# Kernel optimization log

Measured on AMD Instinct MI355X. Metric: run time of the kernel, lower is better.

The kernel has to match this reference:

```python
import jax, jax.numpy as jnp
import numpy as np

B = 262144
N_FEAT = 256
N_D = 64
N_A = 64
N_OUT = N_D + N_A  # 128
N_STEPS = 3
N_STEP_DEP = 2
VBS = 1024
GAMMA = 1.3
EPS_BN = 1e-5
SQRT_HALF = float(np.sqrt(0.5))


def _xavier(key, shape):
    fan_in, fan_out = shape[-2], shape[-1]
    return (jax.random.normal(key, shape) * np.sqrt(2.0 / (fan_in + fan_out))).astype(jnp.float32)


def setup_inputs() -> dict:
    key = jax.random.key(0)
    ks = jax.random.split(key, 8)
    return {
        "x": jax.random.normal(ks[0], (B, N_FEAT), dtype=jnp.float32),
        "bn0_g": jnp.ones((N_FEAT,), jnp.float32),
        "bn0_b": jnp.zeros((N_FEAT,), jnp.float32),
        "W_sh0": _xavier(ks[1], (N_FEAT, 2 * N_OUT)),
        "g_sh0": jnp.ones((2 * N_OUT,), jnp.float32),
        "b_sh0": jnp.zeros((2 * N_OUT,), jnp.float32),
        "W_sh1": _xavier(ks[2], (N_OUT, 2 * N_OUT)),
        "g_sh1": jnp.ones((2 * N_OUT,), jnp.float32),
        "b_sh1": jnp.zeros((2 * N_OUT,), jnp.float32),
        "W_step": _xavier(ks[3], (N_STEPS, N_STEP_DEP, N_OUT, 2 * N_OUT)),
        "g_step": jnp.ones((N_STEPS, N_STEP_DEP, 2 * N_OUT), jnp.float32),
        "b_step": jnp.zeros((N_STEPS, N_STEP_DEP, 2 * N_OUT), jnp.float32),
        "W_att": _xavier(ks[4], (N_STEPS, N_A, N_FEAT)),
        "g_att": jnp.ones((N_STEPS, N_FEAT), jnp.float32),
        "b_att": jnp.zeros((N_STEPS, N_FEAT), jnp.float32),
    }


def batch_norm(x, g, b):
    # training-mode BN over the full batch (biased variance, as torch)
    mu = x.mean(0)
    var = ((x - mu) ** 2).mean(0)
    return (x - mu) * jax.lax.rsqrt(var + EPS_BN) * g + b


def ghost_bn(x, g, b):
    # split batch into virtual sub-batches of VBS and BN each chunk
    n, f = x.shape
    xr = x.reshape(n // VBS, VBS, f)
    mu = xr.mean(1, keepdims=True)
    var = ((xr - mu) ** 2).mean(1, keepdims=True)
    xn = (xr - mu) * jax.lax.rsqrt(var + EPS_BN)
    return xn.reshape(n, f) * g + b


def sparsemax(z):
    zs = jnp.flip(jnp.sort(z, axis=-1), axis=-1)      # descending
    cs = jnp.cumsum(zs, axis=-1)
    n = z.shape[-1]
    k = jnp.arange(1, n + 1, dtype=z.dtype)
    support = (k * zs > cs - 1.0).astype(z.dtype)
    kz = support.sum(-1, keepdims=True)
    idx = jnp.clip(kz - 1.0, 0.0).astype(jnp.int32)
    tau = (jnp.take_along_axis(cs, idx, axis=-1) - 1.0) / kz
    return jnp.maximum(z - tau, 0.0)


def glu(x, W, g, b):
    h = ghost_bn(x @ W, g, b)
    h1, h2 = jnp.split(h, 2, axis=-1)
    return h1 * jax.nn.sigmoid(h2)


def feat_transformer(x, W_sh0, g_sh0, b_sh0, W_sh1, g_sh1, b_sh1, Wst, gst, bst):
    h = glu(x, W_sh0, g_sh0, b_sh0)
    h = (h + glu(h, W_sh1, g_sh1, b_sh1)) * SQRT_HALF
    for j in range(N_STEP_DEP):
        h = (h + glu(h, Wst[j], gst[j], bst[j])) * SQRT_HALF
    return h


def reference(x, bn0_g, bn0_b, W_sh0, g_sh0, b_sh0, W_sh1, g_sh1, b_sh1,
              W_step, g_step, b_step, W_att, g_att, b_att):
    x_bn = batch_norm(x, bn0_g, bn0_b)
    prior = jnp.ones((B, N_FEAT), x.dtype)
    h_a = jnp.zeros((B, N_A), x.dtype)
    d_out = jnp.zeros((B, N_D), x.dtype)
    sl = jnp.asarray(0.0, x.dtype)
    masks = []
    for s in range(N_STEPS):
        a = ghost_bn(h_a @ W_att[s], g_att[s], b_att[s])
        M = sparsemax(prior * a)
        masks.append(M)
        prior = prior * (GAMMA - M)
        h = feat_transformer(M * x_bn, W_sh0, g_sh0, b_sh0, W_sh1, g_sh1, b_sh1,
                             W_step[s], g_step[s], b_step[s])
        d_out = d_out + jax.nn.relu(h[:, :N_D])
        h_a = h[:, N_D:]
        sl = sl + (-M * jnp.log(M + 1e-15)).mean()
    sl = sl / N_STEPS
    return d_out, sl, jnp.stack(masks)
```

## Files before the change

kernel.cpp:

```cpp
#include <hip/hip_runtime.h>
#include <math.h>

#define B_ROWS 262144
#define GAMMA_C 1.3f
#define EPS_C 1e-5f
#define SQH_C 0.70710678118654752440f
#define SL_SCALE (1.0f/201326592.0f)

typedef _Float16 f16;
typedef f16 f16x8 __attribute__((ext_vector_type(8)));
typedef f16 f16x4 __attribute__((ext_vector_type(4)));
typedef float f32x4 __attribute__((ext_vector_type(4)));

__device__ __forceinline__ int SWZ(int row, int kb, int RB, int MSK) {
  return row * RB + (kb ^ ((row & MSK) << 4));
}

__global__ void bn0_accum(const float* __restrict__ x, float* __restrict__ sums) {
  const int col = threadIdx.x;
  const size_t r0 = (size_t)blockIdx.x * 128;
  float s1 = 0.f, s2 = 0.f;
  for (int i = 0; i < 128; ++i) {
    float v = x[(r0 + i) * 256 + col];
    s1 += v; s2 += v * v;
  }
  atomicAdd(&sums[col * 2], s1);
  atomicAdd(&sums[col * 2 + 1], s2);
}

__global__ void bn0_final(const float* __restrict__ sums, const float* __restrict__ g,
                          const float* __restrict__ b, float* __restrict__ bnA,
                          float* __restrict__ bnB) {
  int c = threadIdx.x;
  float mu = sums[c * 2] * (1.f / B_ROWS);
  float var = sums[c * 2 + 1] * (1.f / B_ROWS) - mu * mu;
  float a = rsqrtf(var + EPS_C) * g[c];
  bnA[c] = a;
  bnB[c] = b[c] - mu * a;
}

__global__ void wprep(const float* __restrict__ src, f16* __restrict__ dst, int K) {
  int idx = blockIdx.x * 256 + threadIdx.x;
  int n = idx / K, k = idx - n * K;
  dst[idx] = (f16)src[(size_t)k * 256 + n];
}

__global__ void m0_kernel(const float* __restrict__ ba, float* __restrict__ m0v,
                          float* __restrict__ prior1v, float* __restrict__ slpart) {
  const int l = threadIdx.x;
  const int c0 = l << 2;
  float z[4];
#pragma unroll
  for (int j = 0; j < 4; ++j) z[j] = ba[c0 + j];
  float m = fmaxf(fmaxf(z[0], z[1]), fmaxf(z[2], z[3]));
#pragma unroll
  for (int d = 1; d < 64; d <<= 1) m = fmaxf(m, __shfl_xor(m, d));
  float lo = m - 1.f, hi = m;
  for (int it = 0; it < 24; ++it) {
    float tau = 0.5f * (lo + hi);
    float s = fmaxf(z[0] - tau, 0.f) + fmaxf(z[1] - tau, 0.f) +
              fmaxf(z[2] - tau, 0.f) + fmaxf(z[3] - tau, 0.f);
#pragma unroll
    for (int d = 1; d < 64; d <<= 1) s += __shfl_xor(s, d);
    if (s > 1.f) lo = tau; else hi = tau;
  }
  const float tau = 0.5f * (lo + hi);
  float ent = 0.f;
#pragma unroll
  for (int j = 0; j < 4; ++j) {
    float M = fmaxf(z[j] - tau, 0.f);
    m0v[c0 + j] = M;
    prior1v[c0 + j] = GAMMA_C - M;
    ent -= M * __logf(M + 1e-15f);
  }
#pragma unroll
  for (int d = 1; d < 64; d <<= 1) ent += __shfl_xor(ent, d);
  if (l == 0) slpart[512] = ent * (262144.f * SL_SCALE);
}

__global__ void mx0_kernel(const float* __restrict__ x, const float* __restrict__ m0v,
                           const float* __restrict__ bnA, const float* __restrict__ bnB,
                           float* __restrict__ mk, f16* __restrict__ Mx) {
  __shared__ float sm[256], sa[256], sb[256];
  const int tid = threadIdx.x;
  sm[tid] = m0v[tid]; sa[tid] = bnA[tid]; sb[tid] = bnB[tid];
  __syncthreads();
  const size_t r = (size_t)blockIdx.x * 8 + (tid >> 5);
  const int c0 = (tid & 31) << 3;
  const float* xp = x + r * 256 + c0;
  f32x4 x0 = *(const f32x4*)xp;
  f32x4 x1 = *(const f32x4*)(xp + 4);
  float* mp = mk + r * 256 + c0;
  f16x8 mxv;
#pragma unroll
  for (int j = 0; j < 4; ++j) {
    mp[j] = sm[c0 + j];
    mp[4 + j] = sm[c0 + 4 + j];
    mxv[j] = (f16)(sm[c0 + j] * (x0[j] * sa[c0 + j] + sb[c0 + j]));
    mxv[4 + j] = (f16)(sm[c0 + 4 + j] * (x1[j] * sa[c0 + 4 + j] + sb[c0 + 4 + j]));
  }
  *(f16x8*)(Mx + r * 256 + c0) = mxv;
}

template <int KD, int RESID, int DOUT>
__launch_bounds__(1024, 4)
__global__ void fglu(const f16* __restrict__ Ag, const f16* __restrict__ Wt,
                     const float* __restrict__ gv, const float* __restrict__ bv,
                     f16* __restrict__ ho, float* __restrict__ dout, int s) {
  constexpr int KS = KD / 32;
  constexpr int RB = KD * 2;
  constexpr int MSK = (RB / 16 - 1) < 31 ? (RB / 16 - 1) : 31;
  constexpr int SPT = (KD == 256) ? 2 : 1;
  constexpr int TPR = KD / 8;
  __shared__ __align__(16) f16 sA[64 * KD];
  __shared__ float sS1[512], sS2[512], sAf[256], sBf[256];
  char* sAc = (char*)sA;
  const int tid = threadIdx.x;
  const int w = tid >> 6, l = tid & 63, lg = l >> 4, lc = l & 15;
  const int mw = w >> 3, nw = w & 7;
  const int c1 = nw * 16 + lc, c2 = c1 + 128;
  const int r0 = blockIdx.x << 10;

  f16x8 bf0[KS], bf1[KS];
#pragma unroll
  for (int ks = 0; ks < KS; ++ks) {
    bf0[ks] = *(const f16x8*)(Wt + (size_t)c1 * KD + ks * 32 + lg * 8);
    bf1[ks] = *(const f16x8*)(Wt + (size_t)c2 * KD + ks * 32 + lg * 8);
  }

  f16x8 pv[SPT];
  auto LDA = [&](int ch) {
#pragma unroll
    for (int p = 0; p < SPT; ++p) {
      int flat = p * 1024 + tid;
      int row = flat / TPR, kc = flat % TPR;
      pv[p] = *(const f16x8*)(Ag + (size_t)(r0 + ch * 64 + row) * KD + kc * 8);
    }
  };
  auto STA = [&]() {
#pragma unroll
    for (int p = 0; p < SPT; ++p) {
      int flat = p * 1024 + tid;
      int row = flat / TPR, kc = flat % TPR;
      *(f16x8*)(sAc + SWZ(row, kc * 16, RB, MSK)) = pv[p];
    }
  };

  float st1a = 0.f, st2a = 0.f, st1b = 0.f, st2b = 0.f;
  LDA(0);
  for (int ch = 0; ch < 16; ++ch) {
    __syncthreads();
    STA();
    __syncthreads();
    if (ch < 15) LDA(ch + 1);
#pragma unroll
    for (int mt = 0; mt < 2; ++mt) {
      f32x4 a0 = {0.f,0.f,0.f,0.f}, a1 = {0.f,0.f,0.f,0.f};
      const int ar = mw * 32 + mt * 16 + lc;
#pragma unroll
      for (int ks = 0; ks < KS; ++ks) {
        f16x8 af = *(const f16x8*)(sAc + SWZ(ar, ks * 64 + lg * 16, RB, MSK));
        a0 = __builtin_amdgcn_mfma_f32_16x16x32_f16(af, bf0[ks], a0, 0, 0, 0);
        a1 = __builtin_amdgcn_mfma_f32_16x16x32_f16(af, bf1[ks], a1, 0, 0, 0);
      }
#pragma unroll
      for (int j = 0; j < 4; ++j) {
        st1a += a0[j]; st2a += a0[j] * a0[j];
        st1b += a1[j]; st2b += a1[j] * a1[j];
      }
    }
  }
  st1a += __shfl_xor(st1a, 16); st1a += __shfl_xor(st1a, 32);
  st2a += __shfl_xor(st2a, 16); st2a += __shfl_xor(st2a, 32);
  st1b += __shfl_xor(st1b, 16); st1b += __shfl_xor(st1b, 32);
  st2b += __shfl_xor(st2b, 16); st2b += __shfl_xor(st2b, 32);
  if (l < 16) {
    sS1[mw * 256 + c1] = st1a; sS2[mw * 256 + c1] = st2a;
    sS1[mw * 256 + c2] = st1b; sS2[mw * 256 + c2] = st2b;
  }
  __syncthreads();
  if (tid < 256) {
    float s1 = sS1[tid] + sS1[256 + tid];
    float s2 = sS2[tid] + sS2[256 + tid];
    float mu = s1 * (1.f / 1024.f);
    float var = s2 * (1.f / 1024.f) - mu * mu;
    float a = rsqrtf(var + EPS_C) * gv[tid];
    sAf[tid] = a; sBf[tid] = bv[tid] - mu * a;
  }
  __syncthreads();
  const float bA1 = sAf[c1], bO1 = sBf[c1], bA2 = sAf[c2], bO2 = sBf[c2];

  LDA(0);
  for (int ch = 0; ch < 16; ++ch) {
    __syncthreads();
    STA();
    __syncthreads();
    if (ch < 15) LDA(ch + 1);
#pragma unroll
    for (int mt = 0; mt < 2; ++mt) {
      f32x4 a0 = {0.f,0.f,0.f,0.f}, a1 = {0.f,0.f,0.f,0.f};
      const int ar = mw * 32 + mt * 16 + lc;
#pragma unroll
      for (int ks = 0; ks < KS; ++ks) {
        f16x8 af = *(const f16x8*)(sAc + SWZ(ar, ks * 64 + lg * 16, RB, MSK));
        a0 = __builtin_amdgcn_mfma_f32_16x16x32_f16(af, bf0[ks], a0, 0, 0, 0);
        a1 = __builtin_amdgcn_mfma_f32_16x16x32_f16(af, bf1[ks], a1, 0, 0, 0);
      }
#pragma unroll
      for (int j = 0; j < 4; ++j) {
        float g1 = a0[j] * bA1 + bO1;
        float g2 = a1[j] * bA2 + bO2;
        float hv = g1 / (1.f + __expf(-g2));
        const int rl = mw * 32 + mt * 16 + lg * 4 + j;
        if (RESID) {
          f16 hp = *(const f16*)(sAc + SWZ(rl, c1 * 2, RB, MSK));
          hv = (hv + (float)hp) * SQH_C;
        }
        if (DOUT && nw < 4) {
          float rv = fmaxf(hv, 0.f);
          float* dp = dout + (size_t)(r0 + ch * 64 + rl) * 64 + c1;
          if (s == 0) *dp = rv; else *dp += rv;
        }
        ho[(size_t)(r0 + ch * 64 + rl) * 128 + c1] = (f16)hv;
      }
    }
  }
}

template <int SMODE>
__launch_bounds__(512)
__global__ void attmask(const f16* __restrict__ h1, const f16* __restrict__ Wt,
                        const float* __restrict__ ga, const float* __restrict__ ba,
                        const float* __restrict__ bnA, const float* __restrict__ bnB,
                        const float* __restrict__ prior1v, const f16* __restrict__ prin,
                        f16* __restrict__ prout, const float* __restrict__ x,
                        float* __restrict__ mk, f16* __restrict__ Mx,
                        float* __restrict__ slpart) {
  __shared__ f16 sW[256 * 64];
  __shared__ f16 sA[128 * 64];
  __shared__ float sS1[256], sS2[256], sAf[256], sBf[256], sbA[256], sbB[256], spv[256];
  __shared__ float sEnt[8];
  char* sWc = (char*)sW;
  char* sAc = (char*)sA;
  const int tid = threadIdx.x;
  const int vb = blockIdx.x;
  const int r0 = vb << 10;
  const int w = tid >> 6, l = tid & 63, lc = l & 15, lg = l >> 4;
  if (tid < 256) {
    sS1[tid] = 0.f; sS2[tid] = 0.f;
    sbA[tid] = bnA[tid]; sbB[tid] = bnB[tid];
    if (SMODE == 1) spv[tid] = prior1v[tid];
  }
#pragma unroll
  for (int it = 0; it < 4; ++it) {
    int flat = it * 512 + tid;
    int rw = flat >> 3, kc = flat & 7;
    *(f16x8*)(sWc + SWZ(rw, kc * 16, 128, 7)) = *(const f16x8*)(Wt + rw * 64 + kc * 8);
  }
  const int arow = tid >> 3, akc = tid & 7;
  const f16* aB = h1 + (size_t)(r0 + arow) * 128 + 64 + akc * 8;
  float ent = 0.f;

  for (int pass = 0; pass < 2; ++pass) {
    float st1[16], st2[16];
#pragma unroll
    for (int t = 0; t < 16; ++t) { st1[t] = 0.f; st2[t] = 0.f; }
    f16x8 pv0 = *(const f16x8*)(aB);
    f16x8 pv1 = *(const f16x8*)(aB + (size_t)64 * 128);
    for (int ch = 0; ch < 8; ++ch) {
      __syncthreads();
      *(f16x8*)(sAc + SWZ(arow, akc * 16, 128, 7)) = pv0;
      *(f16x8*)(sAc + SWZ(arow + 64, akc * 16, 128, 7)) = pv1;
      __syncthreads();
      if (ch + 1 < 8) {
        pv0 = *(const f16x8*)(aB + (size_t)(ch + 1) * 128 * 128);
        pv1 = *(const f16x8*)(aB + (size_t)((ch + 1) * 128 + 64) * 128);
      }
      f16x8 af0 = *(const f16x8*)(sAc + SWZ(w * 16 + lc, lg * 16, 128, 7));
      f16x8 af1 = *(const f16x8*)(sAc + SWZ(w * 16 + lc, 64 + lg * 16, 128, 7));
      const int rb = r0 + ch * 128 + w * 16;
      f32x4 z[16];
#pragma unroll
      for (int t = 0; t < 16; ++t) {
        f16x8 b0 = *(const f16x8*)(sWc + SWZ(t * 16 + lc, lg * 16, 128, 7));
        f16x8 b1 = *(const f16x8*)(sWc + SWZ(t * 16 + lc, 64 + lg * 16, 128, 7));
        f32x4 acc = {0.f, 0.f, 0.f, 0.f};
        acc = __builtin_amdgcn_mfma_f32_16x16x32_f16(af0, b0, acc, 0, 0, 0);
        acc = __builtin_amdgcn_mfma_f32_16x16x32_f16(af1, b1, acc, 0, 0, 0);
        if (pass == 0) {
          float s1 = 0.f, s2 = 0.f;
#pragma unroll
          for (int j = 0; j < 4; ++j) { float v = acc[j]; s1 += v; s2 += v * v; }
          st1[t] += s1; st2[t] += s2;
        } else {
          const int c = t * 16 + lc;
          const float a = sAf[c], bb = sBf[c];
#pragma unroll
          for (int j = 0; j < 4; ++j) {
            float pr;
            if (SMODE == 1) pr = spv[c];
            else pr = (float)prin[(size_t)(rb + lg * 4 + j) * 256 + c];
            z[t][j] = (acc[j] * a + bb) * pr;
          }
        }
      }
      if (pass == 1) {
        f32x4 mj, lo, hi;
#pragma unroll
        for (int j = 0; j < 4; ++j) {
          float m = z[0][j];
#pragma unroll
          for (int t = 1; t < 16; ++t) m = fmaxf(m, z[t][j]);
          mj[j] = m;
        }
#pragma unroll
        for (int d = 1; d < 16; d <<= 1)
#pragma unroll
          for (int j = 0; j < 4; ++j) mj[j] = fmaxf(mj[j], __shfl_xor(mj[j], d));
#pragma unroll
        for (int j = 0; j < 4; ++j) { lo[j] = mj[j] - 1.f; hi[j] = mj[j]; }
        for (int itb = 0; itb < 20; ++itb) {
          f32x4 tau, sv;
#pragma unroll
          for (int j = 0; j < 4; ++j) { tau[j] = 0.5f * (lo[j] + hi[j]); sv[j] = 0.f; }
#pragma unroll
          for (int t = 0; t < 16; ++t)
#pragma unroll
            for (int j = 0; j < 4; ++j) sv[j] += fmaxf(z[t][j] - tau[j], 0.f);
#pragma unroll
          for (int d = 1; d < 16; d <<= 1)
#pragma unroll
            for (int j = 0; j < 4; ++j) sv[j] += __shfl_xor(sv[j], d);
#pragma unroll
          for (int j = 0; j < 4; ++j) { if (sv[j] > 1.f) lo[j] = tau[j]; else hi[j] = tau[j]; }
        }
        f32x4 tau;
#pragma unroll
        for (int j = 0; j < 4; ++j) tau[j] = 0.5f * (lo[j] + hi[j]);
#pragma unroll
        for (int t = 0; t < 16; ++t) {
          const int c = t * 16 + lc;
#pragma unroll
          for (int j = 0; j < 4; ++j) {
            const size_t r = (size_t)(rb + lg * 4 + j);
            float Mv = fmaxf(z[t][j] - tau[j], 0.f);
            mk[r * 256 + c] = Mv;
            ent -= Mv * __logf(Mv + 1e-15f);
            float xb = x[r * 256 + c] * sbA[c] + sbB[c];
            Mx[r * 256 + c] = (f16)(Mv * xb);
            if (SMODE == 1) prout[r * 256 + c] = (f16)(spv[c] * (GAMMA_C - Mv));
          }
        }
      }
    }
    if (pass == 0) {
#pragma unroll
      for (int t = 0; t < 16; ++t) {
        float v1 = st1[t], v2 = st2[t];
        v1 += __shfl_xor(v1, 16); v2 += __shfl_xor(v2, 16);
        v1 += __shfl_xor(v1, 32); v2 += __shfl_xor(v2, 32);
        if (l < 16) {
          atomicAdd(&sS1[t * 16 + lc], v1);
          atomicAdd(&sS2[t * 16 + lc], v2);
        }
      }
      __syncthreads();
      if (tid < 256) {
        float mu = sS1[tid] * (1.f / 1024.f);
        float var = sS2[tid] * (1.f / 1024.f) - mu * mu;
        float a = rsqrtf(var + EPS_C) * ga[tid];
        sAf[tid] = a;
        sBf[tid] = ba[tid] - mu * a;
      }
      __syncthreads();
    }
  }
#pragma unroll
  for (int d = 1; d < 64; d <<= 1) ent += __shfl_xor(ent, d);
  if (l == 0) sEnt[w] = ent;
  __syncthreads();
  if (tid == 0) {
    float t = 0.f;
#pragma unroll
    for (int i = 0; i < 8; ++i) t += sEnt[i];
    slpart[(SMODE - 1) * 256 + vb] = t * SL_SCALE;
  }
}

__global__ void sl_reduce(const float* __restrict__ part, float* __restrict__ out, int n) {
  __shared__ float sm[256];
  float s = 0.f;
  for (int i = threadIdx.x; i < n; i += 256) s += part[i];
  sm[threadIdx.x] = s;
  __syncthreads();
  for (int d = 128; d > 0; d >>= 1) {
    if ((int)threadIdx.x < d) sm[threadIdx.x] += sm[threadIdx.x + d];
    __syncthreads();
  }
  if (threadIdx.x == 0) out[0] = sm[0];
}

extern "C" void kernel_launch(void* const* d_in, const int* in_sizes, int n_in,
                              void* d_out, int out_size, void* d_ws, size_t ws_size,
                              hipStream_t stream) {
  (void)in_sizes; (void)n_in; (void)out_size; (void)ws_size;
  const float* x    = (const float*)d_in[0];
  const float* bn0g = (const float*)d_in[1];
  const float* bn0b = (const float*)d_in[2];
  const float* Wsh0 = (const float*)d_in[3];
  const float* gsh0 = (const float*)d_in[4];
  const float* bsh0 = (const float*)d_in[5];
  const float* Wsh1 = (const float*)d_in[6];
  const float* gsh1 = (const float*)d_in[7];
  const float* bsh1 = (const float*)d_in[8];
  const float* Wstep = (const float*)d_in[9];
  const float* gstep = (const float*)d_in[10];
  const float* bstep = (const float*)d_in[11];
  const float* Watt = (const float*)d_in[12];
  const float* gatt = (const float*)d_in[13];
  const float* batt = (const float*)d_in[14];

  float* dout = (float*)d_out;
  float* slo = dout + (size_t)B_ROWS * 64;
  float* masks = slo + 1;

  char* ws = (char*)d_ws;
  size_t off = 0;
  auto carve = [&](size_t bytes) -> char* {
    char* p = ws + off;
    off += (bytes + 255) & ~(size_t)255;
    return p;
  };
  f16* wt_att   = (f16*)carve((size_t)3 * 256 * 64 * 2);
  f16* wt_sh0   = (f16*)carve((size_t)256 * 256 * 2);
  f16* wt_sh1   = (f16*)carve((size_t)256 * 128 * 2);
  f16* wt_step  = (f16*)carve((size_t)6 * 256 * 128 * 2);
  float* bn0sum = (float*)carve(512 * 4);
  float* bnA    = (float*)carve(256 * 4);
  float* bnB    = (float*)carve(256 * 4);
  float* m0v    = (float*)carve(256 * 4);
  float* prior1v= (float*)carve(256 * 4);
  float* slpart = (float*)carve(513 * 4);
  f16* prior    = (f16*)carve((size_t)B_ROWS * 256 * 2);
  f16* Mx       = (f16*)carve((size_t)B_ROWS * 256 * 2);
  f16* h0       = (f16*)carve((size_t)B_ROWS * 128 * 2);
  f16* h1       = (f16*)carve((size_t)B_ROWS * 128 * 2);

  hipMemsetAsync(bn0sum, 0, 512 * 4, stream);
  bn0_accum<<<2048, 256, 0, stream>>>(x, bn0sum);
  bn0_final<<<1, 256, 0, stream>>>(bn0sum, bn0g, bn0b, bnA, bnB);
  for (int s = 1; s < 3; ++s)
    wprep<<<64, 256, 0, stream>>>(Watt + (size_t)s * 64 * 256, wt_att + (size_t)s * 256 * 64, 64);
  wprep<<<256, 256, 0, stream>>>(Wsh0, wt_sh0, 256);
  wprep<<<128, 256, 0, stream>>>(Wsh1, wt_sh1, 128);
  for (int i = 0; i < 6; ++i)
    wprep<<<128, 256, 0, stream>>>(Wstep + (size_t)i * 128 * 256, wt_step + (size_t)i * 256 * 128, 128);
  m0_kernel<<<1, 64, 0, stream>>>(batt, m0v, prior1v, slpart);
  mx0_kernel<<<B_ROWS / 8, 256, 0, stream>>>(x, m0v, bnA, bnB, masks, Mx);

  for (int s = 0; s < 3; ++s) {
    if (s == 1)
      attmask<1><<<256, 512, 0, stream>>>(h1, wt_att + (size_t)1 * 256 * 64,
                                          gatt + 256, batt + 256, bnA, bnB,
                                          prior1v, nullptr, prior, x,
                                          masks + (size_t)1 * B_ROWS * 256, Mx, slpart);
    else if (s == 2)
      attmask<2><<<256, 512, 0, stream>>>(h1, wt_att + (size_t)2 * 256 * 64,
                                          gatt + 512, batt + 512, bnA, bnB,
                                          nullptr, prior, nullptr, x,
                                          masks + (size_t)2 * B_ROWS * 256, Mx, slpart);
    fglu<256, 0, 0><<<256, 1024, 0, stream>>>(Mx, wt_sh0, gsh0, bsh0, h0, nullptr, s);
    fglu<128, 1, 0><<<256, 1024, 0, stream>>>(h0, wt_sh1, gsh1, bsh1, h1, nullptr, s);
    fglu<128, 1, 0><<<256, 1024, 0, stream>>>(h1, wt_step + (size_t)(s * 2 + 0) * 256 * 128,
                                              gstep + (s * 2 + 0) * 256, bstep + (s * 2 + 0) * 256,
                                              h0, nullptr, s);
    fglu<128, 1, 1><<<256, 1024, 0, stream>>>(h0, wt_step + (size_t)(s * 2 + 1) * 256 * 128,
                                              gstep + (s * 2 + 1) * 256, bstep + (s * 2 + 1) * 256,
                                              h1, dout, s);
  }
  sl_reduce<<<1, 256, 0, stream>>>(slpart, slo, 513);
}
```

Baseline: 1.908 ms.

## Compute next layer's ghost-BN statistics in producer kernel, eliminating stats pass

Each GLU/attention kernel previously ran its GEMM twice: once to gather per-virtual-batch BN statistics, then again to normalise. Now the producing kernel keeps its output tile in LDS, runs the next layer's GEMM on it, and writes per-block sum and sum-of-squares to a stats buffer. The consumer reads those stats and needs only one GEMM pass, which removes a full re-read of activations per layer. The cost is extra LDS use and extra next-layer MFMA work with weights loaded from global memory in the producer. The weight-prep launches are also merged into one kernel, and a stored fp16 x_bn replaces recomputing it from x.

```diff
diff --git a/kernel.cpp b/kernel.cpp
--- a/kernel.cpp
+++ b/kernel.cpp
@@ -9,7 +9,6 @@
 
 typedef _Float16 f16;
 typedef f16 f16x8 __attribute__((ext_vector_type(8)));
-typedef f16 f16x4 __attribute__((ext_vector_type(4)));
 typedef float f32x4 __attribute__((ext_vector_type(4)));
 
 __device__ __forceinline__ int SWZ(int row, int kb, int RB, int MSK) {
@@ -39,8 +38,17 @@
   bnB[c] = b[c] - mu * a;
 }
 
-__global__ void wprep(const float* __restrict__ src, f16* __restrict__ dst, int K) {
-  int idx = blockIdx.x * 256 + threadIdx.x;
+__global__ void wprep_all(const float* __restrict__ Wsh0, const float* __restrict__ Wsh1,
+                          const float* __restrict__ Wstep, const float* __restrict__ Watt,
+                          f16* __restrict__ wt_sh0, f16* __restrict__ wt_sh1,
+                          f16* __restrict__ wt_step, f16* __restrict__ wt_att) {
+  int b = blockIdx.x;
+  const float* src; f16* dst; int K, lb;
+  if (b < 256)       { src = Wsh0; dst = wt_sh0; K = 256; lb = b; }
+  else if (b < 384)  { src = Wsh1; dst = wt_sh1; K = 128; lb = b - 256; }
+  else if (b < 1152) { int i = (b - 384) >> 7; src = Wstep + i * 32768; dst = wt_step + i * 32768; K = 128; lb = (b - 384) & 127; }
+  else               { int i = (b - 1152) >> 6; src = Watt + (size_t)(i + 1) * 16384; dst = wt_att + (size_t)(i + 1) * 16384; K = 64; lb = (b - 1152) & 63; }
+  int idx = lb * 256 + threadIdx.x;
   int n = idx / K, k = idx - n * K;
   dst[idx] = (f16)src[(size_t)k * 256 + n];
 }
@@ -78,56 +86,128 @@
   if (l == 0) slpart[512] = ent * (262144.f * SL_SCALE);
 }
 
-__global__ void mx0_kernel(const float* __restrict__ x, const float* __restrict__ m0v,
-                           const float* __restrict__ bnA, const float* __restrict__ bnB,
-                           float* __restrict__ mk, f16* __restrict__ Mx) {
-  __shared__ float sm[256], sa[256], sb[256];
+__launch_bounds__(1024, 4)
+__global__ void mx0(const float* __restrict__ x, const float* __restrict__ m0v,
+                    const float* __restrict__ bnA, const float* __restrict__ bnB,
+                    const f16* __restrict__ Wn, float* __restrict__ mk,
+                    f16* __restrict__ xbn, f16* __restrict__ Mx,
+                    float* __restrict__ stOut) {
+  __shared__ __align__(16) f16 sMx[64 * 256];
+  __shared__ float sm[256], sa[256], sb[256], sS1[512], sS2[512];
+  char* sMc = (char*)sMx;
   const int tid = threadIdx.x;
-  sm[tid] = m0v[tid]; sa[tid] = bnA[tid]; sb[tid] = bnB[tid];
+  const int w = tid >> 6, l = tid & 63, lg = l >> 4, lc = l & 15;
+  const int mw = w >> 3, nw = w & 7;
+  const int c1 = nw * 16 + lc, c2 = c1 + 128;
+  const int vb = blockIdx.x;
+  const int r0 = vb << 10;
+  if (tid < 256) { sm[tid] = m0v[tid]; sa[tid] = bnA[tid]; sb[tid] = bnB[tid]; }
   __syncthreads();
-  const size_t r = (size_t)blockIdx.x * 8 + (tid >> 5);
-  const int c0 = (tid & 31) << 3;
-  const float* xp = x + r * 256 + c0;
-  f32x4 x0 = *(const f32x4*)xp;
-  f32x4 x1 = *(const f32x4*)(xp + 4);
-  float* mp = mk + r * 256 + c0;
-  f16x8 mxv;
-#pragma unroll
-  for (int j = 0; j < 4; ++j) {
-    mp[j] = sm[c0 + j];
-    mp[4 + j] = sm[c0 + 4 + j];
-    mxv[j] = (f16)(sm[c0 + j] * (x0[j] * sa[c0 + j] + sb[c0 + j]));
-    mxv[4 + j] = (f16)(sm[c0 + 4 + j] * (x1[j] * sa[c0 + 4 + j] + sb[c0 + 4 + j]));
-  }
-  *(f16x8*)(Mx + r * 256 + c0) = mxv;
-}
-
-template <int KD, int RESID, int DOUT>
+  float sn1a = 0.f, sn2a = 0.f, sn1b = 0.f, sn2b = 0.f;
+  const int rloc = tid >> 4;
+  const int c0 = (tid & 15) << 4;
+  for (int ch = 0; ch < 16; ++ch) {
+    __syncthreads();
+    const size_t rg = (size_t)(r0 + ch * 64 + rloc);
+    f32x4 xv[4];
+#pragma unroll
+    for (int q = 0; q < 4; ++q) xv[q] = *(const f32x4*)(x + rg * 256 + c0 + q * 4);
+    f16x8 xb2[2], mx2[2];
+    float* mp = mk + rg * 256 + c0;
+#pragma unroll
+    for (int k = 0; k < 16; ++k) {
+      float xbv = xv[k >> 2][k & 3] * sa[c0 + k] + sb[c0 + k];
+      float mxv = sm[c0 + k] * xbv;
+      xb2[k >> 3][k & 7] = (f16)xbv;
+      mx2[k >> 3][k & 7] = (f16)mxv;
+      mp[k] = sm[c0 + k];
+    }
+    *(f16x8*)(xbn + rg * 256 + c0) = xb2[0];
+    *(f16x8*)(xbn + rg * 256 + c0 + 8) = xb2[1];
+    *(f16x8*)(Mx + rg * 256 + c0) = mx2[0];
+    *(f16x8*)(Mx + rg * 256 + c0 + 8) = mx2[1];
+    *(f16x8*)(sMc + SWZ(rloc, c0 * 2, 512, 31)) = mx2[0];
+    *(f16x8*)(sMc + SWZ(rloc, c0 * 2 + 16, 512, 31)) = mx2[1];
+    __syncthreads();
+#pragma unroll
+    for (int mt = 0; mt < 2; ++mt) {
+      f32x4 a0 = {0.f,0.f,0.f,0.f}, a1 = {0.f,0.f,0.f,0.f};
+      const int ar = mw * 32 + mt * 16 + lc;
+#pragma unroll
+      for (int ks = 0; ks < 8; ++ks) {
+        f16x8 af = *(const f16x8*)(sMc + SWZ(ar, ks * 64 + lg * 16, 512, 31));
+        f16x8 w0 = *(const f16x8*)(Wn + (size_t)c1 * 256 + ks * 32 + lg * 8);
+        f16x8 w1 = *(const f16x8*)(Wn + (size_t)c2 * 256 + ks * 32 + lg * 8);
+        a0 = __builtin_amdgcn_mfma_f32_16x16x32_f16(af, w0, a0, 0, 0, 0);
+        a1 = __builtin_amdgcn_mfma_f32_16x16x32_f16(af, w1, a1, 0, 0, 0);
+      }
+#pragma unroll
+      for (int j = 0; j < 4; ++j) {
+        sn1a += a0[j]; sn2a += a0[j] * a0[j];
+        sn1b += a1[j]; sn2b += a1[j] * a1[j];
+      }
+    }
+  }
+  sn1a += __shfl_xor(sn1a, 16); sn1a += __shfl_xor(sn1a, 32);
+  sn2a += __shfl_xor(sn2a, 16); sn2a += __shfl_xor(sn2a, 32);
+  sn1b += __shfl_xor(sn1b, 16); sn1b += __shfl_xor(sn1b, 32);
+  sn2b += __shfl_xor(sn2b, 16); sn2b += __shfl_xor(sn2b, 32);
+  if (l < 16) {
+    sS1[mw * 256 + c1] = sn1a; sS2[mw * 256 + c1] = sn2a;
+    sS1[mw * 256 + c2] = sn1b; sS2[mw * 256 + c2] = sn2b;
+  }
+  __syncthreads();
+  if (tid < 256) {
+    stOut[((size_t)vb * 256 + tid) * 2] = sS1[tid] + sS1[256 + tid];
+    stOut[((size_t)vb * 256 + tid) * 2 + 1] = sS2[tid] + sS2[256 + tid];
+  }
+}
+
+template <int KD, int RESID, int DOUT, int NEXTK>
 __launch_bounds__(1024, 4)
 __global__ void fglu(const f16* __restrict__ Ag, const f16* __restrict__ Wt,
+                     const f16* __restrict__ Wn, const float* __restrict__ stIn,
+                     float* __restrict__ stOut,
                      const float* __restrict__ gv, const float* __restrict__ bv,
                      f16* __restrict__ ho, float* __restrict__ dout, int s) {
   constexpr int KS = KD / 32;
   constexpr int RB = KD * 2;
   constexpr int MSK = (RB / 16 - 1) < 31 ? (RB / 16 - 1) : 31;
+  constexpr int TPR = KD / 8;
   constexpr int SPT = (KD == 256) ? 2 : 1;
-  constexpr int TPR = KD / 8;
+  constexpr int KSN = NEXTK / 32;
+  constexpr int RBN = (NEXTK > 0) ? NEXTK * 2 : 16;
+  constexpr int MSKN = (NEXTK > 0) ? (NEXTK / 8 - 1) : 0;
   __shared__ __align__(16) f16 sA[64 * KD];
+  __shared__ __align__(16) f16 sH[(NEXTK > 0) ? 64 * NEXTK : 8];
   __shared__ float sS1[512], sS2[512], sAf[256], sBf[256];
   char* sAc = (char*)sA;
+  char* sHc = (char*)sH;
   const int tid = threadIdx.x;
   const int w = tid >> 6, l = tid & 63, lg = l >> 4, lc = l & 15;
   const int mw = w >> 3, nw = w & 7;
   const int c1 = nw * 16 + lc, c2 = c1 + 128;
-  const int r0 = blockIdx.x << 10;
-
+  const int vb = blockIdx.x;
+  const int r0 = vb << 10;
+
+  if (tid < 256) {
+    float s1 = stIn[((size_t)vb * 256 + tid) * 2];
+    float s2 = stIn[((size_t)vb * 256 + tid) * 2 + 1];
+    float mu = s1 * (1.f / 1024.f);
+    float var = s2 * (1.f / 1024.f) - mu * mu;
+    float a = rsqrtf(var + EPS_C) * gv[tid];
+    sAf[tid] = a; sBf[tid] = bv[tid] - mu * a;
+  }
   f16x8 bf0[KS], bf1[KS];
 #pragma unroll
   for (int ks = 0; ks < KS; ++ks) {
     bf0[ks] = *(const f16x8*)(Wt + (size_t)c1 * KD + ks * 32 + lg * 8);
     bf1[ks] = *(const f16x8*)(Wt + (size_t)c2 * KD + ks * 32 + lg * 8);
   }
-
+  __syncthreads();
+  const float bA1 = sAf[c1], bO1 = sBf[c1], bA2 = sAf[c2], bO2 = sBf[c2];
+
+  float sn1a = 0.f, sn2a = 0.f, sn1b = 0.f, sn2b = 0.f;
   f16x8 pv[SPT];
   auto LDA = [&](int ch) {
 #pragma unroll
@@ -145,50 +225,6 @@
       *(f16x8*)(sAc + SWZ(row, kc * 16, RB, MSK)) = pv[p];
     }
   };
-
-  float st1a = 0.f, st2a = 0.f, st1b = 0.f, st2b = 0.f;
-  LDA(0);
-  for (int ch = 0; ch < 16; ++ch) {
-    __syncthreads();
-    STA();
-    __syncthreads();
-    if (ch < 15) LDA(ch + 1);
-#pragma unroll
-    for (int mt = 0; mt < 2; ++mt) {
-      f32x4 a0 = {0.f,0.f,0.f,0.f}, a1 = {0.f,0.f,0.f,0.f};
-      const int ar = mw * 32 + mt * 16 + lc;
-#pragma unroll
-      for (int ks = 0; ks < KS; ++ks) {
-        f16x8 af = *(const f16x8*)(sAc + SWZ(ar, ks * 64 + lg * 16, RB, MSK));
-        a0 = __builtin_amdgcn_mfma_f32_16x16x32_f16(af, bf0[ks], a0, 0, 0, 0);
-        a1 = __builtin_amdgcn_mfma_f32_16x16x32_f16(af, bf1[ks], a1, 0, 0, 0);
-      }
-#pragma unroll
-      for (int j = 0; j < 4; ++j) {
-        st1a += a0[j]; st2a += a0[j] * a0[j];
-        st1b += a1[j]; st2b += a1[j] * a1[j];
-      }
-    }
-  }
-  st1a += __shfl_xor(st1a, 16); st1a += __shfl_xor(st1a, 32);
-  st2a += __shfl_xor(st2a, 16); st2a += __shfl_xor(st2a, 32);
-  st1b += __shfl_xor(st1b, 16); st1b += __shfl_xor(st1b, 32);
-  st2b += __shfl_xor(st2b, 16); st2b += __shfl_xor(st2b, 32);
-  if (l < 16) {
-    sS1[mw * 256 + c1] = st1a; sS2[mw * 256 + c1] = st2a;
-    sS1[mw * 256 + c2] = st1b; sS2[mw * 256 + c2] = st2b;
-  }
-  __syncthreads();
-  if (tid < 256) {
-    float s1 = sS1[tid] + sS1[256 + tid];
-    float s2 = sS2[tid] + sS2[256 + tid];
-    float mu = s1 * (1.f / 1024.f);
-    float var = s2 * (1.f / 1024.f) - mu * mu;
-    float a = rsqrtf(var + EPS_C) * gv[tid];
-    sAf[tid] = a; sBf[tid] = bv[tid] - mu * a;
-  }
-  __syncthreads();
-  const float bA1 = sAf[c1], bO1 = sBf[c1], bA2 = sAf[c2], bO2 = sBf[c2];
 
   LDA(0);
   for (int ch = 0; ch < 16; ++ch) {
@@ -221,8 +257,50 @@
           float* dp = dout + (size_t)(r0 + ch * 64 + rl) * 64 + c1;
           if (s == 0) *dp = rv; else *dp += rv;
         }
-        ho[(size_t)(r0 + ch * 64 + rl) * 128 + c1] = (f16)hv;
-      }
+        f16 hf = (f16)hv;
+        ho[(size_t)(r0 + ch * 64 + rl) * 128 + c1] = hf;
+        if constexpr (NEXTK == 128) {
+          *(f16*)(sHc + SWZ(rl, c1 * 2, RBN, MSKN)) = hf;
+        } else if constexpr (NEXTK == 64) {
+          if (nw >= 4) *(f16*)(sHc + SWZ(rl, (c1 - 64) * 2, RBN, MSKN)) = hf;
+        }
+      }
+    }
+    if constexpr (NEXTK > 0) {
+      __syncthreads();
+#pragma unroll
+      for (int mt = 0; mt < 2; ++mt) {
+        f32x4 a0 = {0.f,0.f,0.f,0.f}, a1 = {0.f,0.f,0.f,0.f};
+        const int ar = mw * 32 + mt * 16 + lc;
+#pragma unroll
+        for (int ks = 0; ks < KSN; ++ks) {
+          f16x8 af = *(const f16x8*)(sHc + SWZ(ar, ks * 64 + lg * 16, RBN, MSKN));
+          f16x8 w0 = *(const f16x8*)(Wn + (size_t)c1 * NEXTK + ks * 32 + lg * 8);
+          f16x8 w1 = *(const f16x8*)(Wn + (size_t)c2 * NEXTK + ks * 32 + lg * 8);
+          a0 = __builtin_amdgcn_mfma_f32_16x16x32_f16(af, w0, a0, 0, 0, 0);
+          a1 = __builtin_amdgcn_mfma_f32_16x16x32_f16(af, w1, a1, 0, 0, 0);
+        }
+#pragma unroll
+        for (int j = 0; j < 4; ++j) {
+          sn1a += a0[j]; sn2a += a0[j] * a0[j];
+          sn1b += a1[j]; sn2b += a1[j] * a1[j];
+        }
+      }
+    }
+  }
+  if constexpr (NEXTK > 0) {
+    sn1a += __shfl_xor(sn1a, 16); sn1a += __shfl_xor(sn1a, 32);
+    sn2a += __shfl_xor(sn2a, 16); sn2a += __shfl_xor(sn2a, 32);
+    sn1b += __shfl_xor(sn1b, 16); sn1b += __shfl_xor(sn1b, 32);
+    sn2b += __shfl_xor(sn2b, 16); sn2b += __shfl_xor(sn2b, 32);
+    if (l < 16) {
+      sS1[mw * 256 + c1] = sn1a; sS2[mw * 256 + c1] = sn2a;
+      sS1[mw * 256 + c2] = sn1b; sS2[mw * 256 + c2] = sn2b;
+    }
+    __syncthreads();
+    if (tid < 256) {
+      stOut[((size_t)vb * 256 + tid) * 2] = sS1[tid] + sS1[256 + tid];
+      stOut[((size_t)vb * 256 + tid) * 2 + 1] = sS2[tid] + sS2[256 + tid];
     }
   }
 }
@@ -230,25 +308,31 @@
 template <int SMODE>
 __launch_bounds__(512)
 __global__ void attmask(const f16* __restrict__ h1, const f16* __restrict__ Wt,
+                        const float* __restrict__ stIn,
                         const float* __restrict__ ga, const float* __restrict__ ba,
-                        const float* __restrict__ bnA, const float* __restrict__ bnB,
                         const float* __restrict__ prior1v, const f16* __restrict__ prin,
-                        f16* __restrict__ prout, const float* __restrict__ x,
+                        f16* __restrict__ prout, const f16* __restrict__ xbn,
                         float* __restrict__ mk, f16* __restrict__ Mx,
+                        const f16* __restrict__ Wn, float* __restrict__ stOut,
                         float* __restrict__ slpart) {
-  __shared__ f16 sW[256 * 64];
-  __shared__ f16 sA[128 * 64];
-  __shared__ float sS1[256], sS2[256], sAf[256], sBf[256], sbA[256], sbB[256], spv[256];
-  __shared__ float sEnt[8];
+  __shared__ __align__(16) f16 sW[256 * 64];
+  __shared__ __align__(16) f16 sA[128 * 64];
+  __shared__ __align__(16) f16 sMx[128 * 256];
+  __shared__ float sAf[256], sBf[256], spv[256], sS1[256], sS2[256], sEnt[8];
   char* sWc = (char*)sW;
   char* sAc = (char*)sA;
+  char* sMc = (char*)sMx;
   const int tid = threadIdx.x;
   const int vb = blockIdx.x;
   const int r0 = vb << 10;
   const int w = tid >> 6, l = tid & 63, lc = l & 15, lg = l >> 4;
   if (tid < 256) {
-    sS1[tid] = 0.f; sS2[tid] = 0.f;
-    sbA[tid] = bnA[tid]; sbB[tid] = bnB[tid];
+    float s1 = stIn[((size_t)vb * 256 + tid) * 2];
+    float s2 = stIn[((size_t)vb * 256 + tid) * 2 + 1];
+    float mu = s1 * (1.f / 1024.f);
+    float var = s2 * (1.f / 1024.f) - mu * mu;
+    float a = rsqrtf(var + EPS_C) * ga[tid];
+    sAf[tid] = a; sBf[tid] = ba[tid] - mu * a;
     if (SMODE == 1) spv[tid] = prior1v[tid];
   }
 #pragma unroll
@@ -259,131 +343,131 @@
   }
   const int arow = tid >> 3, akc = tid & 7;
   const f16* aB = h1 + (size_t)(r0 + arow) * 128 + 64 + akc * 8;
+  const int cw1 = w * 16 + lc, cw2 = cw1 + 128;
   float ent = 0.f;
-
-  for (int pass = 0; pass < 2; ++pass) {
-    float st1[16], st2[16];
-#pragma unroll
-    for (int t = 0; t < 16; ++t) { st1[t] = 0.f; st2[t] = 0.f; }
-    f16x8 pv0 = *(const f16x8*)(aB);
-    f16x8 pv1 = *(const f16x8*)(aB + (size_t)64 * 128);
-    for (int ch = 0; ch < 8; ++ch) {
-      __syncthreads();
-      *(f16x8*)(sAc + SWZ(arow, akc * 16, 128, 7)) = pv0;
-      *(f16x8*)(sAc + SWZ(arow + 64, akc * 16, 128, 7)) = pv1;
-      __syncthreads();
-      if (ch + 1 < 8) {
-        pv0 = *(const f16x8*)(aB + (size_t)(ch + 1) * 128 * 128);
-        pv1 = *(const f16x8*)(aB + (size_t)((ch + 1) * 128 + 64) * 128);
-      }
-      f16x8 af0 = *(const f16x8*)(sAc + SWZ(w * 16 + lc, lg * 16, 128, 7));
-      f16x8 af1 = *(const f16x8*)(sAc + SWZ(w * 16 + lc, 64 + lg * 16, 128, 7));
-      const int rb = r0 + ch * 128 + w * 16;
-      f32x4 z[16];
-#pragma unroll
-      for (int t = 0; t < 16; ++t) {
-        f16x8 b0 = *(const f16x8*)(sWc + SWZ(t * 16 + lc, lg * 16, 128, 7));
-        f16x8 b1 = *(const f16x8*)(sWc + SWZ(t * 16 + lc, 64 + lg * 16, 128, 7));
-        f32x4 acc = {0.f, 0.f, 0.f, 0.f};
-        acc = __builtin_amdgcn_mfma_f32_16x16x32_f16(af0, b0, acc, 0, 0, 0);
-        acc = __builtin_amdgcn_mfma_f32_16x16x32_f16(af1, b1, acc, 0, 0, 0);
-        if (pass == 0) {
-          float s1 = 0.f, s2 = 0.f;
-#pragma unroll
-          for (int j = 0; j < 4; ++j) { float v = acc[j]; s1 += v; s2 += v * v; }
-          st1[t] += s1; st2[t] += s2;
-        } else {
-          const int c = t * 16 + lc;
-          const float a = sAf[c], bb = sBf[c];
-#pragma unroll
-          for (int j = 0; j < 4; ++j) {
-            float pr;
-            if (SMODE == 1) pr = spv[c];
-            else pr = (float)prin[(size_t)(rb + lg * 4 + j) * 256 + c];
-            z[t][j] = (acc[j] * a + bb) * pr;
-          }
-        }
-      }
-      if (pass == 1) {
-        f32x4 mj, lo, hi;
-#pragma unroll
-        for (int j = 0; j < 4; ++j) {
-          float m = z[0][j];
-#pragma unroll
-          for (int t = 1; t < 16; ++t) m = fmaxf(m, z[t][j]);
-          mj[j] = m;
-        }
-#pragma unroll
-        for (int d = 1; d < 16; d <<= 1)
-#pragma unroll
-          for (int j = 0; j < 4; ++j) mj[j] = fmaxf(mj[j], __shfl_xor(mj[j], d));
-#pragma unroll
-        for (int j = 0; j < 4; ++j) { lo[j] = mj[j] - 1.f; hi[j] = mj[j]; }
-        for (int itb = 0; itb < 20; ++itb) {
-          f32x4 tau, sv;
-#pragma unroll
-          for (int j = 0; j < 4; ++j) { tau[j] = 0.5f * (lo[j] + hi[j]); sv[j] = 0.f; }
-#pragma unroll
-          for (int t = 0; t < 16; ++t)
-#pragma unroll
-            for (int j = 0; j < 4; ++j) sv[j] += fmaxf(z[t][j] - tau[j], 0.f);
-#pragma unroll
-          for (int d = 1; d < 16; d <<= 1)
-#pragma unroll
-            for (int j = 0; j < 4; ++j) sv[j] += __shfl_xor(sv[j], d);
-#pragma unroll
-          for (int j = 0; j < 4; ++j) { if (sv[j] > 1.f) lo[j] = tau[j]; else hi[j] = tau[j]; }
-        }
-        f32x4 tau;
-#pragma unroll
-        for (int j = 0; j < 4; ++j) tau[j] = 0.5f * (lo[j] + hi[j]);
-#pragma unroll
-        for (int t = 0; t < 16; ++t) {
-          const int c = t * 16 + lc;
-#pragma unroll
-          for (int j = 0; j < 4; ++j) {
-            const size_t r = (size_t)(rb + lg * 4 + j);
-            float Mv = fmaxf(z[t][j] - tau[j], 0.f);
-            mk[r * 256 + c] = Mv;
-            ent -= Mv * __logf(Mv + 1e-15f);
-            float xb = x[r * 256 + c] * sbA[c] + sbB[c];
-            Mx[r * 256 + c] = (f16)(Mv * xb);
-            if (SMODE == 1) prout[r * 256 + c] = (f16)(spv[c] * (GAMMA_C - Mv));
-          }
-        }
-      }
-    }
-    if (pass == 0) {
-#pragma unroll
-      for (int t = 0; t < 16; ++t) {
-        float v1 = st1[t], v2 = st2[t];
-        v1 += __shfl_xor(v1, 16); v2 += __shfl_xor(v2, 16);
-        v1 += __shfl_xor(v1, 32); v2 += __shfl_xor(v2, 32);
-        if (l < 16) {
-          atomicAdd(&sS1[t * 16 + lc], v1);
-          atomicAdd(&sS2[t * 16 + lc], v2);
-        }
-      }
-      __syncthreads();
-      if (tid < 256) {
-        float mu = sS1[tid] * (1.f / 1024.f);
-        float var = sS2[tid] * (1.f / 1024.f) - mu * mu;
-        float a = rsqrtf(var + EPS_C) * ga[tid];
-        sAf[tid] = a;
-        sBf[tid] = ba[tid] - mu * a;
-      }
-      __syncthreads();
+  float sn1a = 0.f, sn2a = 0.f, sn1b = 0.f, sn2b = 0.f;
+  f16x8 pv0 = *(const f16x8*)(aB);
+  f16x8 pv1 = *(const f16x8*)(aB + (size_t)64 * 128);
+  for (int ch = 0; ch < 8; ++ch) {
+    __syncthreads();
+    *(f16x8*)(sAc + SWZ(arow, akc * 16, 128, 7)) = pv0;
+    *(f16x8*)(sAc + SWZ(arow + 64, akc * 16, 128, 7)) = pv1;
+    __syncthreads();
+    if (ch + 1 < 8) {
+      pv0 = *(const f16x8*)(aB + (size_t)(ch + 1) * 128 * 128);
+      pv1 = *(const f16x8*)(aB + (size_t)((ch + 1) * 128 + 64) * 128);
+    }
+    f16x8 af0 = *(const f16x8*)(sAc + SWZ(w * 16 + lc, lg * 16, 128, 7));
+    f16x8 af1 = *(const f16x8*)(sAc + SWZ(w * 16 + lc, 64 + lg * 16, 128, 7));
+    const int rb = r0 + ch * 128 + w * 16;
+    f32x4 z[16];
+#pragma unroll
+    for (int t = 0; t < 16; ++t) {
+      f16x8 b0 = *(const f16x8*)(sWc + SWZ(t * 16 + lc, lg * 16, 128, 7));
+      f16x8 b1 = *(const f16x8*)(sWc + SWZ(t * 16 + lc, 64 + lg * 16, 128, 7));
+      f32x4 acc = {0.f, 0.f, 0.f, 0.f};
+      acc = __builtin_amdgcn_mfma_f32_16x16x32_f16(af0, b0, acc, 0, 0, 0);
+      acc = __builtin_amdgcn_mfma_f32_16x16x32_f16(af1, b1, acc, 0, 0, 0);
+      const int c = t * 16 + lc;
+      const float a = sAf[c], bb = sBf[c];
+#pragma unroll
+      for (int j = 0; j < 4; ++j) {
+        float pr;
+        if (SMODE == 1) pr = spv[c];
+        else pr = (float)prin[(size_t)(rb + lg * 4 + j) * 256 + c];
+        z[t][j] = (acc[j] * a + bb) * pr;
+      }
+    }
+    f32x4 mj, lo, hi;
+#pragma unroll
+    for (int j = 0; j < 4; ++j) {
+      float m = z[0][j];
+#pragma unroll
+      for (int t = 1; t < 16; ++t) m = fmaxf(m, z[t][j]);
+      mj[j] = m;
+    }
+#pragma unroll
+    for (int d = 1; d < 16; d <<= 1)
+#pragma unroll
+      for (int j = 0; j < 4; ++j) mj[j] = fmaxf(mj[j], __shfl_xor(mj[j], d));
+#pragma unroll
+    for (int j = 0; j < 4; ++j) { lo[j] = mj[j] - 1.f; hi[j] = mj[j]; }
+    for (int itb = 0; itb < 20; ++itb) {
+      f32x4 tau, sv;
+#pragma unroll
+      for (int j = 0; j < 4; ++j) { tau[j] = 0.5f * (lo[j] + hi[j]); sv[j] = 0.f; }
+#pragma unroll
+      for (int t = 0; t < 16; ++t)
+#pragma unroll
+        for (int j = 0; j < 4; ++j) sv[j] += fmaxf(z[t][j] - tau[j], 0.f);
+#pragma unroll
+      for (int d = 1; d < 16; d <<= 1)
+#pragma unroll
+        for (int j = 0; j < 4; ++j) sv[j] += __shfl_xor(sv[j], d);
+#pragma unroll
+      for (int j = 0; j < 4; ++j) { if (sv[j] > 1.f) lo[j] = tau[j]; else hi[j] = tau[j]; }
+    }
+    f32x4 tau;
+#pragma unroll
+    for (int j = 0; j < 4; ++j) tau[j] = 0.5f * (lo[j] + hi[j]);
+#pragma unroll
+    for (int t = 0; t < 16; ++t) {
+      const int c = t * 16 + lc;
+#pragma unroll
+      for (int j = 0; j < 4; ++j) {
+        const size_t r = (size_t)(rb + lg * 4 + j);
+        const int rlocal = w * 16 + lg * 4 + j;
+        float Mv = fmaxf(z[t][j] - tau[j], 0.f);
+        mk[r * 256 + c] = Mv;
+        ent -= Mv * __logf(Mv + 1e-15f);
+        float xbv = (float)xbn[r * 256 + c];
+        f16 mxf = (f16)(Mv * xbv);
+        Mx[r * 256 + c] = mxf;
+        *(f16*)(sMc + SWZ(rlocal, c * 2, 512, 31)) = mxf;
+        if (SMODE == 1) prout[r * 256 + c] = (f16)(spv[c] * (GAMMA_C - Mv));
+      }
+    }
+    __syncthreads();
+#pragma unroll
+    for (int mt2 = 0; mt2 < 8; ++mt2) {
+      f32x4 a0 = {0.f,0.f,0.f,0.f}, a1 = {0.f,0.f,0.f,0.f};
+      const int ar2 = mt2 * 16 + lc;
+#pragma unroll
+      for (int ks = 0; ks < 8; ++ks) {
+        f16x8 af = *(const f16x8*)(sMc + SWZ(ar2, ks * 64 + lg * 16, 512, 31));
+        f16x8 w0 = *(const f16x8*)(Wn + (size_t)cw1 * 256 + ks * 32 + lg * 8);
+        f16x8 w1 = *(const f16x8*)(Wn + (size_t)cw2 * 256 + ks * 32 + lg * 8);
+        a0 = __builtin_amdgcn_mfma_f32_16x16x32_f16(af, w0, a0, 0, 0, 0);
+        a1 = __builtin_amdgcn_mfma_f32_16x16x32_f16(af, w1, a1, 0, 0, 0);
+      }
+#pragma unroll
+      for (int j = 0; j < 4; ++j) {
+        sn1a += a0[j]; sn2a += a0[j] * a0[j];
+        sn1b += a1[j]; sn2b += a1[j] * a1[j];
+      }
     }
   }
 #pragma unroll
   for (int d = 1; d < 64; d <<= 1) ent += __shfl_xor(ent, d);
   if (l == 0) sEnt[w] = ent;
+  sn1a += __shfl_xor(sn1a, 16); sn1a += __shfl_xor(sn1a, 32);
+  sn2a += __shfl_xor(sn2a, 16); sn2a += __shfl_xor(sn2a, 32);
+  sn1b += __shfl_xor(sn1b, 16); sn1b += __shfl_xor(sn1b, 32);
+  sn2b += __shfl_xor(sn2b, 16); sn2b += __shfl_xor(sn2b, 32);
+  if (l < 16) {
+    sS1[cw1] = sn1a; sS2[cw1] = sn2a;
+    sS1[cw2] = sn1b; sS2[cw2] = sn2b;
+  }
   __syncthreads();
   if (tid == 0) {
     float t = 0.f;
 #pragma unroll
     for (int i = 0; i < 8; ++i) t += sEnt[i];
     slpart[(SMODE - 1) * 256 + vb] = t * SL_SCALE;
+  }
+  if (tid < 256) {
+    stOut[((size_t)vb * 256 + tid) * 2] = sS1[tid];
+    stOut[((size_t)vb * 256 + tid) * 2 + 1] = sS2[tid];
   }
 }
 
@@ -441,42 +525,55 @@
   float* m0v    = (float*)carve(256 * 4);
   float* prior1v= (float*)carve(256 * 4);
   float* slpart = (float*)carve(513 * 4);
+  float* st_sh0 = (float*)carve((size_t)256 * 256 * 2 * 4);
+  float* st_sh1 = (float*)carve((size_t)256 * 256 * 2 * 4);
+  float* st_st0 = (float*)carve((size_t)256 * 256 * 2 * 4);
+  float* st_st1 = (float*)carve((size_t)256 * 256 * 2 * 4);
+  float* st_att = (float*)carve((size_t)256 * 256 * 2 * 4);
   f16* prior    = (f16*)carve((size_t)B_ROWS * 256 * 2);
   f16* Mx       = (f16*)carve((size_t)B_ROWS * 256 * 2);
+  f16* xbn      = (f16*)carve((size_t)B_ROWS * 256 * 2);
   f16* h0       = (f16*)carve((size_t)B_ROWS * 128 * 2);
   f16* h1       = (f16*)carve((size_t)B_ROWS * 128 * 2);
 
   hipMemsetAsync(bn0sum, 0, 512 * 4, stream);
   bn0_accum<<<2048, 256, 0, stream>>>(x, bn0sum);
   bn0_final<<<1, 256, 0, stream>>>(bn0sum, bn0g, bn0b, bnA, bnB);
-  for (int s = 1; s < 3; ++s)
-    wprep<<<64, 256, 0, stream>>>(Watt + (size_t)s * 64 * 256, wt_att + (size_t)s * 256 * 64, 64);
-  wprep<<<256, 256, 0, stream>>>(Wsh0, wt_sh0, 256);
-  wprep<<<128, 256, 0, stream>>>(Wsh1, wt_sh1, 128);
-  for (int i = 0; i < 6; ++i)
-    wprep<<<128, 256, 0, stream>>>(Wstep + (size_t)i * 128 * 256, wt_step + (size_t)i * 256 * 128, 128);
+  wprep_all<<<1280, 256, 0, stream>>>(Wsh0, Wsh1, Wstep, Watt, wt_sh0, wt_sh1, wt_step, wt_att);
   m0_kernel<<<1, 64, 0, stream>>>(batt, m0v, prior1v, slpart);
-  mx0_kernel<<<B_ROWS / 8, 256, 0, stream>>>(x, m0v, bnA, bnB, masks, Mx);
+  mx0<<<256, 1024, 0, stream>>>(x, m0v, bnA, bnB, wt_sh0, masks, xbn, Mx, st_sh0);
 
   for (int s = 0; s < 3; ++s) {
     if (s == 1)
-      attmask<1><<<256, 512, 0, stream>>>(h1, wt_att + (size_t)1 * 256 * 64,
-                                          gatt + 256, batt + 256, bnA, bnB,
-                                          prior1v, nullptr, prior, x,
-                                          masks + (size_t)1 * B_ROWS * 256, Mx, slpart);
+      attmask<1><<<256, 512, 0, stream>>>(h1, wt_att + (size_t)1 * 256 * 64, st_att,
+                                          gatt + 256, batt + 256, prior1v, nullptr, prior,
+                                          xbn, masks + (size_t)1 * B_ROWS * 256, Mx,
+                                          wt_sh0, st_sh0, slpart);
     else if (s == 2)
-      attmask<2><<<256, 512, 0, stream>>>(h1, wt_att + (size_t)2 * 256 * 64,
-                                          gatt + 512, batt + 512, bnA, bnB,
-                                          nullptr, prior, nullptr, x,
-                                          masks + (size_t)2 * B_ROWS * 256, Mx, slpart);
-    fglu<256, 0, 0><<<256, 1024, 0, stream>>>(Mx, wt_sh0, gsh0, bsh0, h0, nullptr, s);
-    fglu<128, 1, 0><<<256, 1024, 0, stream>>>(h0, wt_sh1, gsh1, bsh1, h1, nullptr, s);
-    fglu<128, 1, 0><<<256, 1024, 0, stream>>>(h1, wt_step + (size_t)(s * 2 + 0) * 256 * 128,
-                                              gstep + (s * 2 + 0) * 256, bstep + (s * 2 + 0) * 256,
-                                              h0, nullptr, s);
-    fglu<128, 1, 1><<<256, 1024, 0, stream>>>(h0, wt_step + (size_t)(s * 2 + 1) * 256 * 128,
-                                              gstep + (s * 2 + 1) * 256, bstep + (s * 2 + 1) * 256,
-                                              h1, dout, s);
+      attmask<2><<<256, 512, 0, stream>>>(h1, wt_att + (size_t)2 * 256 * 64, st_att,
+                                          gatt + 512, batt + 512, nullptr, prior, nullptr,
+                                          xbn, masks + (size_t)2 * B_ROWS * 256, Mx,
+                                          wt_sh0, st_sh0, slpart);
+    fglu<256, 0, 0, 128><<<256, 1024, 0, stream>>>(Mx, wt_sh0, wt_sh1, st_sh0, st_sh1,
+                                                   gsh0, bsh0, h0, nullptr, s);
+    fglu<128, 1, 0, 128><<<256, 1024, 0, stream>>>(h0, wt_sh1, wt_step + (size_t)(s * 2) * 256 * 128,
+                                                   st_sh1, st_st0, gsh1, bsh1, h1, nullptr, s);
+    fglu<128, 1, 0, 128><<<256, 1024, 0, stream>>>(h1, wt_step + (size_t)(s * 2) * 256 * 128,
+                                                   wt_step + (size_t)(s * 2 + 1) * 256 * 128,
+                                                   st_st0, st_st1,
+                                                   gstep + (s * 2) * 256, bstep + (s * 2) * 256,
+                                                   h0, nullptr, s);
+    if (s < 2)
+      fglu<128, 1, 1, 64><<<256, 1024, 0, stream>>>(h0, wt_step + (size_t)(s * 2 + 1) * 256 * 128,
+                                                    wt_att + (size_t)(s + 1) * 256 * 64,
+                                                    st_st1, st_att,
+                                                    gstep + (s * 2 + 1) * 256, bstep + (s * 2 + 1) * 256,
+                                                    h1, dout, s);
+    else
+      fglu<128, 1, 1, 0><<<256, 1024, 0, stream>>>(h0, wt_step + (size_t)(s * 2 + 1) * 256 * 128,
+                                                   nullptr, st_st1, nullptr,
+                                                   gstep + (s * 2 + 1) * 256, bstep + (s * 2 + 1) * 256,
+                                                   h1, dout, s);
   }
   sl_reduce<<<1, 256, 0, stream>>>(slpart, slo, 513);
 }
```

Result: slower. 2.904 ms (+52.2%).
